# Kernel optimization log

Measured on AMD Instinct MI355X. Metric: run time of the kernel, lower is better.

Reference implementation:

```python
import jax, jax.numpy as jnp
import numpy as np

N_NODES = 50000
N_EDGES = 800000
D_IN = 64
D_OUT = 64


def setup_inputs() -> dict:
    key = jax.random.key(0)
    k1, k2, k3, k4 = jax.random.split(key, 4)
    x = jax.random.normal(k1, (N_NODES, D_IN), dtype=jnp.float32)
    edge_index = jax.random.randint(k2, (2, N_EDGES), 0, N_NODES, dtype=jnp.int64)
    scale = np.sqrt(1.0 / D_IN).astype(np.float32)
    W_msg = jax.random.normal(k3, (D_OUT, D_IN), dtype=jnp.float32) * scale
    W_self = jax.random.normal(k4, (D_OUT, D_IN), dtype=jnp.float32) * scale
    b_msg = jnp.zeros((D_OUT,), dtype=jnp.float32)
    b_self = jnp.zeros((D_OUT,), dtype=jnp.float32)
    return {"x": x, "edge_index": edge_index, "W_msg": W_msg, "b_msg": b_msg,
            "W_self": W_self, "b_self": b_self}


def reference(x, edge_index, W_msg, b_msg, W_self, b_self):
    row, col = edge_index[0], edge_index[1]
    n = x.shape[0]
    # message projection on all source nodes, then gather per edge
    msgs_src = x @ W_msg.T + b_msg            # [N, D_OUT]
    per_edge = msgs_src[row]                  # [E, D_OUT] gather
    # scatter-mean into destination nodes
    summed = jax.ops.segment_sum(per_edge, col, num_segments=n)          # [N, D_OUT]
    counts = jax.ops.segment_sum(jnp.ones_like(col, dtype=x.dtype), col,
                                 num_segments=n)                         # [N]
    agg = summed / jnp.maximum(counts, 1.0)[:, None]
    self_out = x @ W_self.T + b_self
    return self_out + agg
```

## Files before the change

kernel.cpp:

```cpp
#include <hip/hip_runtime.h>

constexpr int N_NODES = 50000;
constexpr int N_EDGES = 800000;
constexpr int D = 64;
constexpr int NB = (N_NODES + 63) / 64;
constexpr int BUCKET_CAP = 1792;
constexpr unsigned ZERO_ROW = 50000u;

typedef __attribute__((ext_vector_type(8))) short short8;
typedef __attribute__((ext_vector_type(4))) float f32x4;

static __device__ inline unsigned short f2bf(float f) {
    unsigned u = __float_as_uint(f);
    unsigned r = (u + 0x7FFFu + ((u >> 16) & 1u)) >> 16;
    return (unsigned short)r;
}
static __device__ inline unsigned pack2(float lo, float hi) {
    return (unsigned)f2bf(lo) | ((unsigned)f2bf(hi) << 16);
}
static __device__ inline float bf2f(unsigned short b) {
    return __uint_as_float((unsigned)b << 16);
}

constexpr int BIN_BLOCKS = 256;
constexpr int EDGES_PER_BIN_BLOCK = (N_EDGES + BIN_BLOCKS - 1) / BIN_BLOCKS;

__global__ __launch_bounds__(512) void k_bin_place(
    const float* __restrict__ x, unsigned short* __restrict__ xb,
    const float* __restrict__ W_msg, const float* __restrict__ W_self,
    unsigned short* __restrict__ B_packed,
    const int* __restrict__ edge_index,
    unsigned* __restrict__ g_cursor, unsigned* __restrict__ bucket_data)
{
    __shared__ unsigned ent_sh[EDGES_PER_BIN_BLOCK];
    __shared__ unsigned lcount[NB];
    __shared__ unsigned lbase[NB];

    int tid = threadIdx.x;

    for (int b = tid; b < NB; b += 512) lcount[b] = 0u;

    int gid = blockIdx.x * 512 + tid;
    for (int t = gid; t < N_NODES * D / 4; t += BIN_BLOCKS * 512) {
        float4 v = ((const float4*)x)[t];
        uint2 p;
        p.x = pack2(v.x, v.y);
        p.y = pack2(v.z, v.w);
        ((uint2*)xb)[t] = p;
    }
    if (blockIdx.x == 0) {
        for (int idx = tid; idx < 64 * 128; idx += 512) {
            int n = idx >> 7;
            int k = idx & 127;
            float v = (k < 64) ? W_self[n * 64 + k] : W_msg[n * 64 + (k - 64)];
            B_packed[idx] = f2bf(v);
        }
    } else if (blockIdx.x == 1) {
        if (tid < 8)
            *(uint4*)&xb[ZERO_ROW * D + tid * 8] = make_uint4(0u, 0u, 0u, 0u);
    }

    int e0 = blockIdx.x * EDGES_PER_BIN_BLOCK;
    int e1 = min(e0 + EDGES_PER_BIN_BLOCK, N_EDGES);
    int ne = e1 - e0;
    __syncthreads();

    for (int e = e0 + tid; e < e1; e += 512) {
        int dst = edge_index[N_EDGES + e];
        int src = edge_index[e];
        ent_sh[e - e0] = ((unsigned)src << 16) | (unsigned)dst;
        atomicAdd(&lcount[dst >> 6], 1u);
    }
    __syncthreads();

    for (int b = tid; b < NB; b += 512) {
        unsigned c = lcount[b];
        lbase[b] = c ? ((unsigned)b * BUCKET_CAP + atomicAdd(&g_cursor[b], c)) : 0u;
    }
    __syncthreads();
    for (int b = tid; b < NB; b += 512) lcount[b] = 0u;
    __syncthreads();

    for (int i = tid; i < ne; i += 512) {
        unsigned ent = ent_sh[i];
        unsigned dst = ent & 0xFFFFu;
        unsigned b   = dst >> 6;
        unsigned off = atomicAdd(&lcount[b], 1u);
        bucket_data[lbase[b] + off] = (ent >> 16) | ((dst & 63u) << 16);
    }
}

constexpr int A_STRIDE = 136;

__global__ __launch_bounds__(512) void k_fused(
    const unsigned short* __restrict__ x_bf16,
    const unsigned short* __restrict__ B_packed,
    const float* __restrict__ b_msg, const float* __restrict__ b_self,
    const unsigned* __restrict__ cursor,
    const unsigned* __restrict__ bucket_data,
    float* __restrict__ out)
{
    __shared__ __align__(16) unsigned short A_sh[64 * A_STRIDE];
    __shared__ __align__(16) unsigned short B_sh[64 * A_STRIDE];
    __shared__ unsigned short sorted_sh[BUCKET_CAP];
    __shared__ unsigned cnt_sh[64];
    __shared__ unsigned poff_sh[64];
    __shared__ unsigned woff_sh[64];

    int tid  = threadIdx.x;
    int w    = tid >> 6;
    int lane = tid & 63;
    int r0   = blockIdx.x * 64;

    unsigned start = (unsigned)blockIdx.x * BUCKET_CAP;
    unsigned cnt   = cursor[blockIdx.x];

    if (tid < 64) cnt_sh[tid] = 0u;

    unsigned entr[3];
    int ner = 0;
    for (unsigned i = (unsigned)tid; i < cnt && ner < 3; i += 512u)
        entr[ner++] = bucket_data[start + i];

    for (int idx = tid; idx < 64 * 8; idx += 512) {
        int row = idx >> 3;
        int c   = idx & 7;
        int g   = r0 + row;
        uint4 v = make_uint4(0u, 0u, 0u, 0u);
        if (g < N_NODES) v = *(const uint4*)&x_bf16[g * D + c * 8];
        *(uint4*)&A_sh[row * A_STRIDE + c * 8] = v;
    }
    for (int idx = tid; idx < 64 * 16; idx += 512) {
        int n = idx >> 4;
        int c = idx & 15;
        uint4 v = *(const uint4*)&B_packed[n * 128 + c * 8];
        *(uint4*)&B_sh[n * A_STRIDE + c * 8] = v;
    }
    for (int i = tid; i < BUCKET_CAP; i += 512)
        sorted_sh[i] = (unsigned short)ZERO_ROW;
    __syncthreads();

    #pragma unroll
    for (int q = 0; q < 3; ++q)
        if (q < ner) atomicAdd(&cnt_sh[entr[q] >> 16], 1u);
    for (unsigned i = 3u * 512u + (unsigned)tid; i < cnt; i += 512u)
        atomicAdd(&cnt_sh[bucket_data[start + i] >> 16], 1u);
    __syncthreads();

    if (tid < 64) {
        unsigned c  = cnt_sh[tid];
        unsigned pc = (c + 7u) & ~7u;
        unsigned xsum = pc;
        #pragma unroll
        for (int s = 1; s < 64; s <<= 1) {
            unsigned v = (unsigned)__shfl_up((int)xsum, s);
            if (lane >= s) xsum += v;
        }
        poff_sh[tid] = xsum - pc;
        woff_sh[tid] = xsum - pc;
    }
    __syncthreads();

    #pragma unroll
    for (int q = 0; q < 3; ++q) {
        if (q < ner) {
            unsigned e = entr[q];
            unsigned slot = atomicAdd(&woff_sh[e >> 16], 1u);
            sorted_sh[slot] = (unsigned short)(e & 0xFFFFu);
        }
    }
    for (unsigned i = 3u * 512u + (unsigned)tid; i < cnt; i += 512u) {
        unsigned e = bucket_data[start + i];
        unsigned slot = atomicAdd(&woff_sh[e >> 16], 1u);
        sorted_sh[slot] = (unsigned short)(e & 0xFFFFu);
    }
    __syncthreads();

    int Q = lane >> 4;
    int f = lane & 15;

    #pragma unroll
    for (int pass = 0; pass < 2; ++pass) {
        int lrow = w * 8 + pass * 4 + Q;
        unsigned s0 = poff_sh[lrow];
        unsigned dc = cnt_sh[lrow];
        unsigned pc = (dc + 7u) & ~7u;

        float a0 = 0.f, a1 = 0.f, a2 = 0.f, a3 = 0.f;
        for (unsigned j = 0; j < pc; j += 8u) {
            ushort4 rv[8];
            #pragma unroll
            for (int u = 0; u < 8; ++u) {
                unsigned src = (unsigned)sorted_sh[s0 + j + u];
                rv[u] = *(const ushort4*)&x_bf16[(src << 6) + 4u * (unsigned)f];
            }
            #pragma unroll
            for (int u = 0; u < 8; ++u) {
                a0 += bf2f(rv[u].x); a1 += bf2f(rv[u].y);
                a2 += bf2f(rv[u].z); a3 += bf2f(rv[u].w);
            }
        }
        float inv = dc ? 1.0f / (float)dc : 0.0f;
        uint2 p;
        p.x = pack2(a0 * inv, a1 * inv);
        p.y = pack2(a2 * inv, a3 * inv);
        *(uint2*)&A_sh[lrow * A_STRIDE + 64 + 4 * f] = p;
    }
    __syncthreads();

    int wm   = w & 3;
    int ng   = (w >> 2) * 2;
    int quad = lane >> 4;
    int l15  = lane & 15;

    f32x4 accr[2] = {{0.f,0.f,0.f,0.f},{0.f,0.f,0.f,0.f}};

    #pragma unroll
    for (int k0 = 0; k0 < 128; k0 += 32) {
        short8 a = *(const short8*)&A_sh[(16 * wm + l15) * A_STRIDE + k0 + quad * 8];
        #pragma unroll
        for (int t = 0; t < 2; ++t) {
            short8 b = *(const short8*)&B_sh[(16 * (ng + t) + l15) * A_STRIDE + k0 + quad * 8];
            accr[t] = __builtin_amdgcn_mfma_f32_16x16x32_bf16(a, b, accr[t], 0, 0, 0);
        }
    }

    #pragma unroll
    for (int t = 0; t < 2; ++t) {
        int col = (ng + t) * 16 + l15;
        float bs = b_self[col];
        float bm = b_msg[col];
        #pragma unroll
        for (int r = 0; r < 4; ++r) {
            int lrow = 16 * wm + quad * 4 + r;
            int grow = r0 + lrow;
            if (grow < N_NODES) {
                float vv = accr[t][r] + bs + (cnt_sh[lrow] > 0u ? bm : 0.0f);
                out[grow * D + col] = vv;
            }
        }
    }
}

extern "C" void kernel_launch(void* const* d_in, const int* in_sizes, int n_in,
                              void* d_out, int out_size, void* d_ws, size_t ws_size,
                              hipStream_t stream) {
    const float* x      = (const float*)d_in[0];
    const int*   edges  = (const int*)  d_in[1];
    const float* W_msg  = (const float*)d_in[2];
    const float* b_msg  = (const float*)d_in[3];
    const float* W_self = (const float*)d_in[4];
    const float* b_self = (const float*)d_in[5];
    float*       out    = (float*)d_out;

    char* ws = (char*)d_ws;
    unsigned*       cursor      = (unsigned*)(ws + 0);
    unsigned short* B_packed    = (unsigned short*)(ws + 4096);
    unsigned*       bucket_data = (unsigned*)(ws + 20480);
    unsigned short* x_bf16      = (unsigned short*)(ws + 20480 + (size_t)NB * BUCKET_CAP * 4);

    hipMemsetAsync(cursor, 0, NB * sizeof(unsigned), stream);

    k_bin_place<<<BIN_BLOCKS, 512, 0, stream>>>(x, x_bf16, W_msg, W_self,
                                                B_packed, edges, cursor, bucket_data);
    k_fused<<<NB, 512, 0, stream>>>(x_bf16, B_packed, b_msg, b_self,
                                    cursor, bucket_data, out);
}
```

Before: 111.8 us.

## Replace global atomic bucketing with per-block local sort and segment index

The binning kernel now does a block-local prefix scan over bucket counts, sorts its edges by destination bucket in shared memory, and writes a contiguous per-block segment plus a count/offset table. This removes the global atomic cursors and the cursor memset. The fused kernel then reads up to 256 small segments per bucket, one thread per source block, instead of one contiguous bucket. The trade is that these segment reads are serial per thread, uneven and less coalesced, and the table is scanned in a strided way.

After: 112.3 us. About the same (+0.5%).

```diff
diff --git a/kernel.cpp b/kernel.cpp
--- a/kernel.cpp
+++ b/kernel.cpp
@@ -7,6 +7,11 @@
 constexpr int BUCKET_CAP = 1792;
 constexpr unsigned ZERO_ROW = 50000u;
 
+constexpr int BIN_BLOCKS = 256;
+constexpr int EPB = (N_EDGES + BIN_BLOCKS - 1) / BIN_BLOCKS;
+constexpr int SEG_STRIDE = 3136;
+constexpr int CNT_STRIDE = 784;
+
 typedef __attribute__((ext_vector_type(8))) short short8;
 typedef __attribute__((ext_vector_type(4))) float f32x4;
 
@@ -21,26 +26,28 @@
 static __device__ inline float bf2f(unsigned short b) {
     return __uint_as_float((unsigned)b << 16);
 }
-
-constexpr int BIN_BLOCKS = 256;
-constexpr int EDGES_PER_BIN_BLOCK = (N_EDGES + BIN_BLOCKS - 1) / BIN_BLOCKS;
 
 __global__ __launch_bounds__(512) void k_bin_place(
     const float* __restrict__ x, unsigned short* __restrict__ xb,
     const float* __restrict__ W_msg, const float* __restrict__ W_self,
     unsigned short* __restrict__ B_packed,
     const int* __restrict__ edge_index,
-    unsigned* __restrict__ g_cursor, unsigned* __restrict__ bucket_data)
+    unsigned* __restrict__ cnt2off, unsigned* __restrict__ edge_sorted)
 {
-    __shared__ unsigned ent_sh[EDGES_PER_BIN_BLOCK];
+    __shared__ unsigned ent_sh[EPB];
+    __shared__ unsigned sort_sh[SEG_STRIDE];
     __shared__ unsigned lcount[NB];
-    __shared__ unsigned lbase[NB];
-
-    int tid = threadIdx.x;
+    __shared__ unsigned loff[NB + 2];
+    __shared__ unsigned wsum[8];
+
+    int tid  = threadIdx.x;
+    int w    = tid >> 6;
+    int lane = tid & 63;
+    int blk  = blockIdx.x;
 
     for (int b = tid; b < NB; b += 512) lcount[b] = 0u;
 
-    int gid = blockIdx.x * 512 + tid;
+    int gid = blk * 512 + tid;
     for (int t = gid; t < N_NODES * D / 4; t += BIN_BLOCKS * 512) {
         float4 v = ((const float4*)x)[t];
         uint2 p;
@@ -48,20 +55,20 @@
         p.y = pack2(v.z, v.w);
         ((uint2*)xb)[t] = p;
     }
-    if (blockIdx.x == 0) {
+    if (blk == 0) {
         for (int idx = tid; idx < 64 * 128; idx += 512) {
             int n = idx >> 7;
             int k = idx & 127;
             float v = (k < 64) ? W_self[n * 64 + k] : W_msg[n * 64 + (k - 64)];
             B_packed[idx] = f2bf(v);
         }
-    } else if (blockIdx.x == 1) {
+    } else if (blk == 1) {
         if (tid < 8)
             *(uint4*)&xb[ZERO_ROW * D + tid * 8] = make_uint4(0u, 0u, 0u, 0u);
     }
 
-    int e0 = blockIdx.x * EDGES_PER_BIN_BLOCK;
-    int e1 = min(e0 + EDGES_PER_BIN_BLOCK, N_EDGES);
+    int e0 = blk * EPB;
+    int e1 = min(e0 + EPB, N_EDGES);
     int ne = e1 - e0;
     __syncthreads();
 
@@ -73,21 +80,52 @@
     }
     __syncthreads();
 
-    for (int b = tid; b < NB; b += 512) {
-        unsigned c = lcount[b];
-        lbase[b] = c ? ((unsigned)b * BUCKET_CAP + atomicAdd(&g_cursor[b], c)) : 0u;
-    }
-    __syncthreads();
-    for (int b = tid; b < NB; b += 512) lcount[b] = 0u;
+    {
+        int i0 = 2 * tid, i1 = 2 * tid + 1;
+        unsigned v0 = (i0 < NB) ? lcount[i0] : 0u;
+        unsigned v1 = (i1 < NB) ? lcount[i1] : 0u;
+        unsigned s  = v0 + v1;
+        unsigned xinc = s;
+        #pragma unroll
+        for (int d = 1; d < 64; d <<= 1) {
+            unsigned t = (unsigned)__shfl_up((int)xinc, d);
+            if (lane >= d) xinc += t;
+        }
+        if (lane == 63) wsum[w] = xinc;
+        __syncthreads();
+        if (w == 0 && lane < 8) {
+            unsigned y  = wsum[lane];
+            unsigned yy = y;
+            #pragma unroll
+            for (int d = 1; d < 8; d <<= 1) {
+                unsigned t = (unsigned)__shfl_up((int)yy, d);
+                if (lane >= d) yy += t;
+            }
+            wsum[lane] = yy - y;
+        }
+        __syncthreads();
+        unsigned ex = wsum[w] + (xinc - s);
+        if (i0 < NB) {
+            loff[i0] = ex;
+            cnt2off[blk * CNT_STRIDE + i0] = ex | (v0 << 16);
+        }
+        if (i1 < NB) {
+            loff[i1] = ex + v0;
+            cnt2off[blk * CNT_STRIDE + i1] = (ex + v0) | (v1 << 16);
+        }
+    }
     __syncthreads();
 
     for (int i = tid; i < ne; i += 512) {
-        unsigned ent = ent_sh[i];
-        unsigned dst = ent & 0xFFFFu;
-        unsigned b   = dst >> 6;
-        unsigned off = atomicAdd(&lcount[b], 1u);
-        bucket_data[lbase[b] + off] = (ent >> 16) | ((dst & 63u) << 16);
-    }
+        unsigned ent  = ent_sh[i];
+        unsigned dst  = ent & 0xFFFFu;
+        unsigned pos  = atomicAdd(&loff[dst >> 6], 1u);
+        sort_sh[pos]  = (ent >> 16) | ((dst & 63u) << 16);
+    }
+    __syncthreads();
+
+    for (int i = tid; i < ne; i += 512)
+        edge_sorted[blk * SEG_STRIDE + i] = sort_sh[i];
 }
 
 constexpr int A_STRIDE = 136;
@@ -96,8 +134,8 @@
     const unsigned short* __restrict__ x_bf16,
     const unsigned short* __restrict__ B_packed,
     const float* __restrict__ b_msg, const float* __restrict__ b_self,
-    const unsigned* __restrict__ cursor,
-    const unsigned* __restrict__ bucket_data,
+    const unsigned* __restrict__ cnt2off,
+    const unsigned* __restrict__ edge_sorted,
     float* __restrict__ out)
 {
     __shared__ __align__(16) unsigned short A_sh[64 * A_STRIDE];
@@ -112,16 +150,15 @@
     int lane = tid & 63;
     int r0   = blockIdx.x * 64;
 
-    unsigned start = (unsigned)blockIdx.x * BUCKET_CAP;
-    unsigned cnt   = cursor[blockIdx.x];
+    unsigned scnt = 0u;
+    const unsigned* segp = nullptr;
+    if (tid < 256) {
+        unsigned meta = cnt2off[tid * CNT_STRIDE + blockIdx.x];
+        segp = edge_sorted + tid * SEG_STRIDE + (meta & 0xFFFFu);
+        scnt = meta >> 16;
+    }
 
     if (tid < 64) cnt_sh[tid] = 0u;
-
-    unsigned entr[3];
-    int ner = 0;
-    for (unsigned i = (unsigned)tid; i < cnt && ner < 3; i += 512u)
-        entr[ner++] = bucket_data[start + i];
-
     for (int idx = tid; idx < 64 * 8; idx += 512) {
         int row = idx >> 3;
         int c   = idx & 7;
@@ -140,11 +177,8 @@
         sorted_sh[i] = (unsigned short)ZERO_ROW;
     __syncthreads();
 
-    #pragma unroll
-    for (int q = 0; q < 3; ++q)
-        if (q < ner) atomicAdd(&cnt_sh[entr[q] >> 16], 1u);
-    for (unsigned i = 3u * 512u + (unsigned)tid; i < cnt; i += 512u)
-        atomicAdd(&cnt_sh[bucket_data[start + i] >> 16], 1u);
+    for (unsigned u = 0; u < scnt; ++u)
+        atomicAdd(&cnt_sh[segp[u] >> 16], 1u);
     __syncthreads();
 
     if (tid < 64) {
@@ -161,16 +195,8 @@
     }
     __syncthreads();
 
-    #pragma unroll
-    for (int q = 0; q < 3; ++q) {
-        if (q < ner) {
-            unsigned e = entr[q];
-            unsigned slot = atomicAdd(&woff_sh[e >> 16], 1u);
-            sorted_sh[slot] = (unsigned short)(e & 0xFFFFu);
-        }
-    }
-    for (unsigned i = 3u * 512u + (unsigned)tid; i < cnt; i += 512u) {
-        unsigned e = bucket_data[start + i];
+    for (unsigned u = 0; u < scnt; ++u) {
+        unsigned e = segp[u];
         unsigned slot = atomicAdd(&woff_sh[e >> 16], 1u);
         sorted_sh[slot] = (unsigned short)(e & 0xFFFFu);
     }
@@ -254,15 +280,13 @@
     float*       out    = (float*)d_out;
 
     char* ws = (char*)d_ws;
-    unsigned*       cursor      = (unsigned*)(ws + 0);
-    unsigned short* B_packed    = (unsigned short*)(ws + 4096);
-    unsigned*       bucket_data = (unsigned*)(ws + 20480);
-    unsigned short* x_bf16      = (unsigned short*)(ws + 20480 + (size_t)NB * BUCKET_CAP * 4);
-
-    hipMemsetAsync(cursor, 0, NB * sizeof(unsigned), stream);
+    unsigned short* B_packed    = (unsigned short*)(ws + 0);
+    unsigned*       cnt2off     = (unsigned*)(ws + 16384);
+    unsigned*       edge_sorted = (unsigned*)(ws + 819200);
+    unsigned short* x_bf16      = (unsigned short*)(ws + 4030464);
 
     k_bin_place<<<BIN_BLOCKS, 512, 0, stream>>>(x, x_bf16, W_msg, W_self,
-                                                B_packed, edges, cursor, bucket_data);
+                                                B_packed, edges, cnt2off, edge_sorted);
     k_fused<<<NB, 512, 0, stream>>>(x_bf16, B_packed, b_msg, b_self,
-                                    cursor, bucket_data, out);
-}
+                                    cnt2off, edge_sorted, out);
+}
```
